# Performance work log

Hardware: AMD Instinct MI355X
Metric: run time of the kernel (lower is better)

## Reference

```python
import jax, jax.numpy as jnp
import numpy as np

N, E, D, G = 50000, 600000, 128, 64
EPS = 1e-5


def prelu(x, a):
    return jnp.where(x >= 0, x, a * x)


def degree_norms(edge_src, edge_dst):
    ones = jnp.ones((E,), jnp.float32)
    deg_out = jax.ops.segment_sum(ones, edge_src, num_segments=N)
    deg_in = jax.ops.segment_sum(ones, edge_dst, num_segments=N)
    norm_src = jnp.where(deg_out > 0, jax.lax.rsqrt(jnp.maximum(deg_out, 1.0)), 0.0)
    norm_dst = jnp.where(deg_in > 0, jax.lax.rsqrt(jnp.maximum(deg_in, 1.0)), 0.0)
    return norm_src, norm_dst


def graph_conv(x, W, b, alpha, edge_src, edge_dst, norm_src, norm_dst):
    # DGL GraphConv norm='both': D_out^{-1/2} on src, aggregate, D_in^{-1/2} on dst, then linear
    xs = x * norm_src[:, None]
    agg = jax.ops.segment_sum(xs[edge_src], edge_dst, num_segments=N)
    agg = agg * norm_dst[:, None]
    h = agg @ W + b
    return prelu(h, alpha)


def batch_norm(h, gamma, beta):
    mean = jnp.mean(h, axis=0)
    var = jnp.mean(jnp.square(h - mean), axis=0)
    return (h - mean) * jax.lax.rsqrt(var + EPS) * gamma + beta


def setup_inputs() -> dict:
    key = jax.random.key(0)
    ks = jax.random.split(key, 8)
    inp = {
        "heat": jax.random.normal(ks[0], (N, D), jnp.float32),
        "edge_src": jax.random.randint(ks[1], (E,), 0, N, jnp.int32),
        "edge_dst": jax.random.randint(ks[2], (E,), 0, N, jnp.int32),
        "graph_ids": jnp.sort(jax.random.randint(ks[3], (N,), 0, G, jnp.int32)),
    }
    for i in range(2):
        kw = jax.random.fold_in(ks[4], i)
        inp[f"W{i}"] = jax.random.normal(kw, (D, D), jnp.float32) * (1.0 / np.sqrt(D))
        inp[f"b{i}"] = jnp.zeros((D,), jnp.float32)
        inp[f"ac{i}"] = jnp.float32(0.25)  # conv PReLU alpha
        inp[f"g{i}"] = jnp.ones((D,), jnp.float32)
        inp[f"be{i}"] = jnp.zeros((D,), jnp.float32)
        inp[f"aa{i}"] = jnp.float32(0.25)  # outer PReLU alpha
    return inp


def reference(heat, edge_src, edge_dst, graph_ids,
              W0, b0, ac0, g0, be0, aa0,
              W1, b1, ac1, g1, be1, aa1):
    norm_src, norm_dst = degree_norms(edge_src, edge_dst)
    x = heat  # dropout in eval mode -> identity
    h = graph_conv(x, W0, b0, ac0, edge_src, edge_dst, norm_src, norm_dst)
    h = prelu(batch_norm(h, g0, be0), aa0)
    gh = jax.ops.segment_sum(h, graph_ids, num_segments=G)
    h = graph_conv(h, W1, b1, ac1, edge_src, edge_dst, norm_src, norm_dst)
    h = prelu(batch_norm(h, g1, be1), aa1)
    gh = gh + jax.ops.segment_sum(h, graph_ids, num_segments=G)
    return h, gh
```

## Files before the change

kernel.cpp:

```cpp
#include <hip/hip_runtime.h>
#include <hip/hip_fp8.h>

#define NN 50000
#define NE 600000
#define DD 128
#define GG 64
#define EPS 1e-5f
#define CAP 64
#define HB 60
#define ECHUNK 10000
#define HALF 25000
#define HWORDS 12500
#define ZROW 50000

typedef unsigned short u16;
typedef unsigned int u32;
typedef unsigned char u8;
typedef u16 u16x8 __attribute__((ext_vector_type(8)));
typedef u8 u8x16 __attribute__((ext_vector_type(16)));
typedef u8 u8x8 __attribute__((ext_vector_type(8)));
typedef short bf16x8 __attribute__((ext_vector_type(8)));
typedef float f32x4 __attribute__((ext_vector_type(4)));

__device__ __forceinline__ float bf2f(u16 v) {
    return __uint_as_float(((u32)v) << 16);
}
__device__ __forceinline__ u16 f2bf(float f) {
    u32 u = __float_as_uint(f);
    u += 0x7fff + ((u >> 16) & 1);
    return (u16)(u >> 16);
}
__device__ __forceinline__ float f8tof(u8 b) {
    __hip_fp8_e4m3 v;
    v.__x = b;
    return (float)v;
}
__device__ __forceinline__ u8 ftof8(float f) {
    return __hip_fp8_e4m3(f).__x;
}

__global__ void k_wprep(const float* __restrict__ W0, const float* __restrict__ W1,
                        u16* __restrict__ wtb, int* __restrict__ cnt_in,
                        float* __restrict__ stats , float* __restrict__ gh,
                        u8* __restrict__ xsb) {
    int k = threadIdx.x;
    int c = blockIdx.x;
    int lay = blockIdx.y;
    const float* W = lay ? W1 : W0;
    wtb[lay * DD * DD + c * DD + k] = f2bf(W[k * DD + c]);

    int gtid = (blockIdx.y * gridDim.x + blockIdx.x) * DD + threadIdx.x;
    for (int i = gtid; i < NN; i += 32768) cnt_in[i] = 0;
    if (gtid < 4 * DD) stats[gtid] = 0.f;
    if (gtid < GG * DD) gh[gtid] = 0.f;
    if (gtid < 16) {
        u8x8 z = {0, 0, 0, 0, 0, 0, 0, 0};
        *(u8x8*)(xsb + (size_t)ZROW * DD + gtid * 8) = z;
    }
}

__global__ __launch_bounds__(256) void k_histbuild(
        const int* __restrict__ src, const int* __restrict__ dst,
        u32* __restrict__ partials, int* __restrict__ cnt_in, u16* __restrict__ csr) {
    __shared__ u32 hc[HWORDS];
    int t = threadIdx.x, b = blockIdx.x, p = blockIdx.y;
    for (int i = t; i < HWORDS; i += 256) hc[i] = 0;
    __syncthreads();
    int e0 = b * ECHUNK;
    int bs = e0 + p * (ECHUNK / 2);
    for (int e = bs + t; e < bs + ECHUNK / 2; e += 256) {
        int d = dst[e];
        int pos = atomicAdd(&cnt_in[d], 1);
        if (pos < CAP) csr[(size_t)d * CAP + pos] = (u16)src[e];
    }
    int lo = p * HALF;
    for (int e = e0 + t; e < e0 + ECHUNK; e += 256) {
        int s = src[e] - lo;
        if ((u32)s < (u32)HALF) atomicAdd(&hc[s >> 1], 1u << ((s & 1) << 4));
    }
    __syncthreads();
    u32* outp = partials + (size_t)(p * HB + b) * HWORDS;
    for (int i = t; i < HWORDS; i += 256) outp[i] = hc[i];
}

__global__ void k_hist_reduce(const u32* __restrict__ partials, const int* __restrict__ cnt_in,
                              float* __restrict__ norm_src, float* __restrict__ norm_dst) {
    int j = blockIdx.x * 256 + threadIdx.x;
    int p = blockIdx.y;
    if (j < HWORDS) {
        u32 s = 0;
#pragma unroll 4
        for (int b = 0; b < HB; ++b) s += partials[(size_t)(p * HB + b) * HWORDS + j];
        int n0 = p * HALF + 2 * j;
        u32 c0 = s & 0xffffu, c1 = s >> 16;
        norm_src[n0]     = c0 ? rsqrtf((float)c0) : 0.f;
        norm_src[n0 + 1] = c1 ? rsqrtf((float)c1) : 0.f;
        int d0 = cnt_in[n0], d1 = cnt_in[n0 + 1];
        norm_dst[n0]     = d0 > 0 ? rsqrtf((float)d0) : 0.f;
        norm_dst[n0 + 1] = d1 > 0 ? rsqrtf((float)d1) : 0.f;
    }
}

__global__ void k_scale_rows(const float* __restrict__ norm_src, const float* __restrict__ x,
                             u8* __restrict__ xsb) {
    int idx = blockIdx.x * 256 + threadIdx.x;
    int row = idx >> 4;
    int c8 = (idx & 15) << 3;
    float ns = norm_src[row];
    const float4* xp = (const float4*)(x + (size_t)row * DD + c8);
    float4 a = xp[0], b = xp[1];
    u8x8 o;
    o[0] = ftof8(a.x * ns); o[1] = ftof8(a.y * ns); o[2] = ftof8(a.z * ns); o[3] = ftof8(a.w * ns);
    o[4] = ftof8(b.x * ns); o[5] = ftof8(b.y * ns); o[6] = ftof8(b.z * ns); o[7] = ftof8(b.w * ns);
    *(u8x8*)(xsb + (size_t)row * DD + c8) = o;
}

#define LOADF8(v, ii)                                                    \
    u8x16 v##0 = *(const u8x16*)(xcol + (size_t)(ii)[0] * DD);           \
    u8x16 v##1 = *(const u8x16*)(xcol + (size_t)(ii)[1] * DD);           \
    u8x16 v##2 = *(const u8x16*)(xcol + (size_t)(ii)[2] * DD);           \
    u8x16 v##3 = *(const u8x16*)(xcol + (size_t)(ii)[3] * DD);           \
    u8x16 v##4 = *(const u8x16*)(xcol + (size_t)(ii)[4] * DD);           \
    u8x16 v##5 = *(const u8x16*)(xcol + (size_t)(ii)[5] * DD);           \
    u8x16 v##6 = *(const u8x16*)(xcol + (size_t)(ii)[6] * DD);           \
    u8x16 v##7 = *(const u8x16*)(xcol + (size_t)(ii)[7] * DD);

#define ACCF8(acc, v)                                                    \
    _Pragma("unroll")                                                    \
    for (int j = 0; j < 16; ++j) {                                       \
        float a01 = f8tof(v##0[j]) + f8tof(v##1[j]);                     \
        float a23 = f8tof(v##2[j]) + f8tof(v##3[j]);                     \
        float a45 = f8tof(v##4[j]) + f8tof(v##5[j]);                     \
        float a67 = f8tof(v##6[j]) + f8tof(v##7[j]);                     \
        acc[j] += (a01 + a23) + (a45 + a67);                             \
    }

__global__ __launch_bounds__(256) void k_gg(
        const u8* __restrict__ xsb, const int* __restrict__ cnt_in,
        const u16* __restrict__ csr, const float* __restrict__ norm_dst,
        const u16* __restrict__ wtb, const float* __restrict__ bias,
        const float* __restrict__ ac, u16* __restrict__ hpreb,
        float* __restrict__ sums, float* __restrict__ sumsq) {
    __shared__ u16 sAg[4][16][DD + 8];
    __shared__ float sStat[2][4][DD];
    int t = threadIdx.x;
    int w = t >> 6;
    int l = t & 63;
    int rb = blockIdx.x * 64 + w * 16;
    bool wvalid = (rb < NN);
    int cl8 = l & 7;
    int rw = l >> 3;
    const u8* xcol = xsb + cl8 * 16;

    if (wvalid) {
#pragma unroll
        for (int gp = 0; gp < 2; ++gp) {
            int r = rb + gp * 8 + rw;
            int cnt = min(cnt_in[r], CAP);
            const u16* ce = csr + (size_t)r * CAP;
            float acc[16];
#pragma unroll
            for (int j = 0; j < 16; ++j) acc[j] = 0.f;
            int e = 0;
            for (; e + 8 <= cnt; e += 8) {
                u16x8 ii = *(const u16x8*)(ce + e);
                LOADF8(va, ii)
                ACCF8(acc, va)
            }
            if (e < cnt) {
                u16x8 ii = *(const u16x8*)(ce + e);
                int jj[8];
#pragma unroll
                for (int j = 0; j < 8; ++j) jj[j] = (e + j < cnt) ? (int)ii[j] : ZROW;
                LOADF8(vm, jj)
                ACCF8(acc, vm)
            }
            float nd = norm_dst[r];
            u16x8 o0, o1;
#pragma unroll
            for (int j = 0; j < 8; ++j) {
                o0[j] = f2bf(acc[j] * nd);
                o1[j] = f2bf(acc[8 + j] * nd);
            }
            *(u16x8*)&sAg[w][gp * 8 + rw][cl8 * 16] = o0;
            *(u16x8*)&sAg[w][gp * 8 + rw][cl8 * 16 + 8] = o1;
        }
    }
    __syncthreads();

    int lr = l & 15;
    int kg = l >> 4;
    float alpha = ac[0];

    bf16x8 afrag[4];
    if (wvalid) {
        const u16* abase = &sAg[w][lr][kg * 8];
        afrag[0] = *(const bf16x8*)(abase);
        afrag[1] = *(const bf16x8*)(abase + 32);
        afrag[2] = *(const bf16x8*)(abase + 64);
        afrag[3] = *(const bf16x8*)(abase + 96);
    }

#pragma unroll
    for (int ct = 0; ct < 8; ++ct) {
        int c = ct * 16;
        float sS = 0.f, sQ = 0.f;
        if (wvalid) {
            const u16* bbase = wtb + (size_t)(c + lr) * DD + kg * 8;
            bf16x8 b0 = *(const bf16x8*)(bbase);
            bf16x8 b1 = *(const bf16x8*)(bbase + 32);
            bf16x8 b2 = *(const bf16x8*)(bbase + 64);
            bf16x8 b3 = *(const bf16x8*)(bbase + 96);
            float bv = bias[c + lr];
            f32x4 acc = {bv, bv, bv, bv};
            acc = __builtin_amdgcn_mfma_f32_16x16x32_bf16(afrag[0], b0, acc, 0, 0, 0);
            acc = __builtin_amdgcn_mfma_f32_16x16x32_bf16(afrag[1], b1, acc, 0, 0, 0);
            acc = __builtin_amdgcn_mfma_f32_16x16x32_bf16(afrag[2], b2, acc, 0, 0, 0);
            acc = __builtin_amdgcn_mfma_f32_16x16x32_bf16(afrag[3], b3, acc, 0, 0, 0);
#pragma unroll
            for (int j = 0; j < 4; ++j) {
                float h = acc[j];
                h = h >= 0.f ? h : alpha * h;
                u16 hb = f2bf(h);
                float hq = bf2f(hb);
                int grow = rb + kg * 4 + j;
                hpreb[(size_t)grow * DD + c + lr] = hb;
                sS += hq;
                sQ += hq * hq;
            }
        }
        sS += __shfl_xor(sS, 16); sS += __shfl_xor(sS, 32);
        sQ += __shfl_xor(sQ, 16); sQ += __shfl_xor(sQ, 32);
        if (kg == 0) {
            sStat[0][w][c + lr] = sS;
            sStat[1][w][c + lr] = sQ;
        }
    }
    __syncthreads();
    if (t < DD) {
        float s = sStat[0][0][t] + sStat[0][1][t] + sStat[0][2][t] + sStat[0][3][t];
        atomicAdd(&sums[t], s);
    } else if (t < 2 * DD) {
        int c = t - DD;
        float q = sStat[1][0][c] + sStat[1][1][c] + sStat[1][2][c] + sStat[1][3][c];
        atomicAdd(&sumsq[c], q);
    }
}

__global__ void k_bn_prelu(const u16* __restrict__ hpreb,
                           const float* __restrict__ sums, const float* __restrict__ sumsq,
                           const float* __restrict__ gamma, const float* __restrict__ beta,
                           const float* __restrict__ aa, const float* __restrict__ nsrc,
                           float* __restrict__ h_out, u8* __restrict__ xs_next, int writeXs) {
    __shared__ float sc[DD], sh[DD];
    int t = threadIdx.x;
    if (t < DD) {
        float mean = sums[t] * (1.0f / NN);
        float var = sumsq[t] * (1.0f / NN) - mean * mean;
        float inv = rsqrtf(var + EPS);
        float s = inv * gamma[t];
        sc[t] = s;
        sh[t] = beta[t] - mean * s;
    }
    __syncthreads();
    int idx = blockIdx.x * 256 + t;
    int row = idx >> 4;
    int c8 = (idx & 15) << 3;
    float a = aa[0];
    u16x8 hv = *(const u16x8*)(hpreb + (size_t)idx * 8);
    float v[8];
#pragma unroll
    for (int j = 0; j < 8; ++j) v[j] = bf2f(hv[j]) * sc[c8 + j] + sh[c8 + j];
#pragma unroll
    for (int j = 0; j < 8; ++j) v[j] = v[j] >= 0.f ? v[j] : a * v[j];
    float4* op = (float4*)(h_out + (size_t)idx * 8);
    op[0] = make_float4(v[0], v[1], v[2], v[3]);
    op[1] = make_float4(v[4], v[5], v[6], v[7]);
    if (writeXs) {
        float ns = nsrc[row];
        u8x8 o;
#pragma unroll
        for (int j = 0; j < 8; ++j) o[j] = ftof8(v[j] * ns);
        *(u8x8*)(xs_next + (size_t)row * DD + c8) = o;
    }
}

__global__ void k_seg(const u16* __restrict__ hpreb, const int* __restrict__ gids,
                      const float* __restrict__ sums, const float* __restrict__ sumsq,
                      const float* __restrict__ gamma, const float* __restrict__ beta,
                      const float* __restrict__ aa, float* __restrict__ gh) {
    __shared__ float red[2][DD];
    __shared__ float sc[DD], sh[DD];
    int t = threadIdx.x;
    if (t < DD) {
        float mean = sums[t] * (1.0f / NN);
        float var = sumsq[t] * (1.0f / NN) - mean * mean;
        float inv = rsqrtf(var + EPS);
        float s = inv * gamma[t];
        sc[t] = s;
        sh[t] = beta[t] - mean * s;
    }
    __syncthreads();
    int g = blockIdx.x;
    int slice = blockIdx.y;
    int lo, hi;
    {
        int l = 0, r = NN;
        while (l < r) { int m = (l + r) >> 1; if (gids[m] < g) l = m + 1; else r = m; }
        lo = l;
        r = NN;
        while (l < r) { int m = (l + r) >> 1; if (gids[m] < g + 1) l = m + 1; else r = m; }
        hi = l;
    }
    int cnt = hi - lo;
    int chunk = (cnt + 7) >> 3;
    int s0 = lo + slice * chunk;
    int s1 = min(s0 + chunk, hi);
    float a = aa[0];
    int c = t & 127;
    int half = t >> 7;
    float s = 0.f;
    for (int row = s0 + half; row < s1; row += 2) {
        float v = bf2f(hpreb[(size_t)row * DD + c]) * sc[c] + sh[c];
        v = v >= 0.f ? v : a * v;
        s += v;
    }
    red[half][c] = s;
    __syncthreads();
    if (t < DD)
        atomicAdd(&gh[g * DD + t], red[0][t] + red[1][t]);
}

extern "C" void kernel_launch(void* const* d_in, const int* in_sizes, int n_in,
                              void* d_out, int out_size, void* d_ws, size_t ws_size,
                              hipStream_t stream) {
    const float* heat = (const float*)d_in[0];
    const int* esrc = (const int*)d_in[1];
    const int* edst = (const int*)d_in[2];
    const int* gids = (const int*)d_in[3];
    const float* Wp[2]  = {(const float*)d_in[4],  (const float*)d_in[10]};
    const float* bp[2]  = {(const float*)d_in[5],  (const float*)d_in[11]};
    const float* acp[2] = {(const float*)d_in[6],  (const float*)d_in[12]};
    const float* gp[2]  = {(const float*)d_in[7],  (const float*)d_in[13]};
    const float* bep[2] = {(const float*)d_in[8],  (const float*)d_in[14]};
    const float* aap[2] = {(const float*)d_in[9],  (const float*)d_in[15]};

    float* out = (float*)d_out;
    float* h_out = out;
    float* gh = out + (size_t)NN * DD;

    char* wsp = (char*)d_ws;
    int* cnt_in_i   = (int*)wsp;              wsp += NN * sizeof(int);
    float* norm_src = (float*)wsp;            wsp += NN * sizeof(float);
    float* norm_dst = (float*)wsp;            wsp += NN * sizeof(float);
    float* stats    = (float*)wsp;            wsp += 4 * DD * sizeof(float);
    u16* wtb        = (u16*)wsp;              wsp += 2 * DD * DD * sizeof(u16);
    u8* xsb         = (u8*)wsp;               wsp += (size_t)(NN + 1) * DD;
    u16* hpreb      = (u16*)wsp;              wsp += (size_t)NN * DD * sizeof(u16);
    u16* csr        = (u16*)wsp;              wsp += (size_t)NN * CAP * sizeof(u16);
    u32* partials   = (u32*)wsp;              wsp += (size_t)2 * HB * HWORDS * sizeof(u32);

    dim3 gwp(DD, 2);
    k_wprep<<<gwp, DD, 0, stream>>>(Wp[0], Wp[1], wtb, cnt_in_i, stats, gh, xsb);
    dim3 ghb(HB, 2);
    k_histbuild<<<ghb, 256, 0, stream>>>(esrc, edst, partials, cnt_in_i, csr);
    dim3 gred((HWORDS + 255) / 256, 2);
    k_hist_reduce<<<gred, 256, 0, stream>>>(partials, cnt_in_i, norm_src, norm_dst);
    k_scale_rows<<<NN * 16 / 256, 256, 0, stream>>>(norm_src, heat, xsb);

    for (int layer = 0; layer < 2; ++layer) {
        float* sums_l  = stats + layer * 2 * DD;
        float* sumsq_l = sums_l + DD;
        k_gg<<<(NN + 63) / 64, 256, 0, stream>>>(xsb, cnt_in_i, csr, norm_dst,
                                                 wtb + layer * DD * DD, bp[layer], acp[layer],
                                                 hpreb, sums_l, sumsq_l);
        k_bn_prelu<<<NN * 16 / 256, 256, 0, stream>>>(hpreb, sums_l, sumsq_l,
                                                      gp[layer], bep[layer], aap[layer],
                                                      norm_src, h_out, xsb, layer == 0 ? 1 : 0);
        dim3 gseg(GG, 8);
        k_seg<<<gseg, 256, 0, stream>>>(hpreb, gids, sums_l, sumsq_l,
                                        gp[layer], bep[layer], aap[layer], gh);
    }
}
```

Before: 225.2 us.

## Build CSR via LDS histogram, prefix offsets and placement instead of global atomics

Replaces the global-atomic CSR bucket fill with a three-pass scheme. First, per-chunk LDS histograms are built for both dst and src. Second, a per-node exclusive scan across chunks yields in-degree and per-chunk base offsets. Third, a placement kernel uses LDS atomics seeded from those offsets to write source ids into the capped CSR slots. This removes contended global atomics on cnt_in, at the cost of an extra kernel launch, a second partials buffer, and rereading the edge arrays. Slot order within each row also becomes deterministic by chunk.

```diff
diff --git a/kernel.cpp b/kernel.cpp
--- a/kernel.cpp
+++ b/kernel.cpp
@@ -40,7 +40,7 @@
 }
 
 __global__ void k_wprep(const float* __restrict__ W0, const float* __restrict__ W1,
-                        u16* __restrict__ wtb, int* __restrict__ cnt_in,
+                        u16* __restrict__ wtb,
                         float* __restrict__ stats , float* __restrict__ gh,
                         u8* __restrict__ xsb) {
     int k = threadIdx.x;
@@ -50,7 +50,6 @@
     wtb[lay * DD * DD + c * DD + k] = f2bf(W[k * DD + c]);
 
     int gtid = (blockIdx.y * gridDim.x + blockIdx.x) * DD + threadIdx.x;
-    for (int i = gtid; i < NN; i += 32768) cnt_in[i] = 0;
     if (gtid < 4 * DD) stats[gtid] = 0.f;
     if (gtid < GG * DD) gh[gtid] = 0.f;
     if (gtid < 16) {
@@ -59,45 +58,79 @@
     }
 }
 
-__global__ __launch_bounds__(256) void k_histbuild(
+__global__ __launch_bounds__(256) void k_histA(
         const int* __restrict__ src, const int* __restrict__ dst,
-        u32* __restrict__ partials, int* __restrict__ cnt_in, u16* __restrict__ csr) {
+        u32* __restrict__ pdst, u32* __restrict__ psrc) {
     __shared__ u32 hc[HWORDS];
-    int t = threadIdx.x, b = blockIdx.x, p = blockIdx.y;
+    int b = blockIdx.x;
+    int p = blockIdx.y & 1;
+    int kind = blockIdx.y >> 1;
+    const int* __restrict__ arr = kind ? src : dst;
+    int t = threadIdx.x;
     for (int i = t; i < HWORDS; i += 256) hc[i] = 0;
     __syncthreads();
+    int lo = p * HALF;
     int e0 = b * ECHUNK;
-    int bs = e0 + p * (ECHUNK / 2);
-    for (int e = bs + t; e < bs + ECHUNK / 2; e += 256) {
-        int d = dst[e];
-        int pos = atomicAdd(&cnt_in[d], 1);
-        if (pos < CAP) csr[(size_t)d * CAP + pos] = (u16)src[e];
-    }
-    int lo = p * HALF;
     for (int e = e0 + t; e < e0 + ECHUNK; e += 256) {
-        int s = src[e] - lo;
-        if ((u32)s < (u32)HALF) atomicAdd(&hc[s >> 1], 1u << ((s & 1) << 4));
-    }
-    __syncthreads();
-    u32* outp = partials + (size_t)(p * HB + b) * HWORDS;
+        int v = arr[e] - lo;
+        if ((u32)v < (u32)HALF) atomicAdd(&hc[v >> 1], 1u << ((v & 1) << 4));
+    }
+    __syncthreads();
+    u32* outp = (kind ? psrc : pdst) + (size_t)(p * HB + b) * HWORDS;
     for (int i = t; i < HWORDS; i += 256) outp[i] = hc[i];
 }
 
-__global__ void k_hist_reduce(const u32* __restrict__ partials, const int* __restrict__ cnt_in,
-                              float* __restrict__ norm_src, float* __restrict__ norm_dst) {
+__global__ void k_off(u32* __restrict__ pdst, const u32* __restrict__ psrc,
+                      int* __restrict__ cnt_in,
+                      float* __restrict__ norm_src, float* __restrict__ norm_dst) {
     int j = blockIdx.x * 256 + threadIdx.x;
     int p = blockIdx.y;
-    if (j < HWORDS) {
-        u32 s = 0;
+    if (j >= HWORDS) return;
+    u32 run0 = 0, run1 = 0;
 #pragma unroll 4
-        for (int b = 0; b < HB; ++b) s += partials[(size_t)(p * HB + b) * HWORDS + j];
-        int n0 = p * HALF + 2 * j;
-        u32 c0 = s & 0xffffu, c1 = s >> 16;
-        norm_src[n0]     = c0 ? rsqrtf((float)c0) : 0.f;
-        norm_src[n0 + 1] = c1 ? rsqrtf((float)c1) : 0.f;
-        int d0 = cnt_in[n0], d1 = cnt_in[n0 + 1];
-        norm_dst[n0]     = d0 > 0 ? rsqrtf((float)d0) : 0.f;
-        norm_dst[n0 + 1] = d1 > 0 ? rsqrtf((float)d1) : 0.f;
+    for (int b = 0; b < HB; ++b) {
+        size_t idx = (size_t)(p * HB + b) * HWORDS + j;
+        u32 w = pdst[idx];
+        pdst[idx] = run0 | (run1 << 16);
+        run0 += w & 0xffffu;
+        run1 += w >> 16;
+    }
+    u32 s0 = 0, s1 = 0;
+#pragma unroll 4
+    for (int b = 0; b < HB; ++b) {
+        u32 w = psrc[(size_t)(p * HB + b) * HWORDS + j];
+        s0 += w & 0xffffu;
+        s1 += w >> 16;
+    }
+    int n0 = p * HALF + 2 * j;
+    cnt_in[n0]     = (int)run0;
+    cnt_in[n0 + 1] = (int)run1;
+    norm_dst[n0]     = run0 ? rsqrtf((float)run0) : 0.f;
+    norm_dst[n0 + 1] = run1 ? rsqrtf((float)run1) : 0.f;
+    norm_src[n0]     = s0 ? rsqrtf((float)s0) : 0.f;
+    norm_src[n0 + 1] = s1 ? rsqrtf((float)s1) : 0.f;
+}
+
+__global__ __launch_bounds__(256) void k_place(
+        const int* __restrict__ src, const int* __restrict__ dst,
+        const u32* __restrict__ pdst, u16* __restrict__ csr) {
+    __shared__ u32 ctr[HWORDS];
+    int b = blockIdx.x, p = blockIdx.y;
+    int t = threadIdx.x;
+    const u32* basep = pdst + (size_t)(p * HB + b) * HWORDS;
+    for (int i = t; i < HWORDS; i += 256) ctr[i] = basep[i];
+    __syncthreads();
+    int lo = p * HALF;
+    int e0 = b * ECHUNK;
+    for (int e = e0 + t; e < e0 + ECHUNK; e += 256) {
+        int d = dst[e];
+        int v = d - lo;
+        if ((u32)v < (u32)HALF) {
+            int sh = (v & 1) << 4;
+            u32 old = atomicAdd(&ctr[v >> 1], 1u << sh);
+            u32 pos = (old >> sh) & 0xffffu;
+            if (pos < CAP) csr[(size_t)d * CAP + pos] = (u16)src[e];
+        }
     }
 }
 
@@ -358,14 +391,17 @@
     u8* xsb         = (u8*)wsp;               wsp += (size_t)(NN + 1) * DD;
     u16* hpreb      = (u16*)wsp;              wsp += (size_t)NN * DD * sizeof(u16);
     u16* csr        = (u16*)wsp;              wsp += (size_t)NN * CAP * sizeof(u16);
-    u32* partials   = (u32*)wsp;              wsp += (size_t)2 * HB * HWORDS * sizeof(u32);
+    u32* pdst       = (u32*)wsp;              wsp += (size_t)2 * HB * HWORDS * sizeof(u32);
+    u32* psrc       = (u32*)wsp;              wsp += (size_t)2 * HB * HWORDS * sizeof(u32);
 
     dim3 gwp(DD, 2);
-    k_wprep<<<gwp, DD, 0, stream>>>(Wp[0], Wp[1], wtb, cnt_in_i, stats, gh, xsb);
-    dim3 ghb(HB, 2);
-    k_histbuild<<<ghb, 256, 0, stream>>>(esrc, edst, partials, cnt_in_i, csr);
-    dim3 gred((HWORDS + 255) / 256, 2);
-    k_hist_reduce<<<gred, 256, 0, stream>>>(partials, cnt_in_i, norm_src, norm_dst);
+    k_wprep<<<gwp, DD, 0, stream>>>(Wp[0], Wp[1], wtb, stats, gh, xsb);
+    dim3 gha(HB, 4);
+    k_histA<<<gha, 256, 0, stream>>>(esrc, edst, pdst, psrc);
+    dim3 goff((HWORDS + 255) / 256, 2);
+    k_off<<<goff, 256, 0, stream>>>(pdst, psrc, cnt_in_i, norm_src, norm_dst);
+    dim3 gpl(HB, 2);
+    k_place<<<gpl, 256, 0, stream>>>(esrc, edst, pdst, csr);
     k_scale_rows<<<NN * 16 / 256, 256, 0, stream>>>(norm_src, heat, xsb);
 
     for (int layer = 0; layer < 2; ++layer) {
```

After: 233.7 us. 3.8% more time.
